# Kernel tuning notes

Hardware: AMD Instinct MI355X
Metric: run time of the kernel (lower is better)

## Reference

```python
import jax, jax.numpy as jnp
import numpy as np

T_STEPS = 30
HIDDEN = 16
INPUT_DIM = 32
OUTPUT_DIM = 1
BATCH = 262144


def setup_inputs() -> dict:
    key = jax.random.key(0)
    ks = jax.random.split(key, 8)
    u = lambda k, shape: jax.random.uniform(k, shape, jnp.float32, -0.25, 0.25)
    return {
        "x": jax.random.normal(ks[0], (BATCH, INPUT_DIM), jnp.float32),
        "T": T_STEPS,
        "W_ih": u(ks[1], (HIDDEN, INPUT_DIM)),
        "W_hh": u(ks[2], (HIDDEN, HIDDEN)),
        "b_ih": u(ks[3], (HIDDEN,)),
        "b_hh": u(ks[4], (HIDDEN,)),
        "W_fc": jax.random.normal(ks[5], (OUTPUT_DIM, HIDDEN), jnp.float32) * 0.25,
        "b_fc": jax.random.normal(ks[6], (OUTPUT_DIM,), jnp.float32) * 0.25,
    }


def reference(x, T, W_ih, W_hh, b_ih, b_hh, W_fc, b_fc):
    # Input is the same at every timestep (x repeated T times), so the
    # input projection is computed once and reused across the scan.
    xproj = x @ W_ih.T + b_ih + b_hh  # [B, H]
    h0 = jnp.zeros((x.shape[0], W_hh.shape[0]), dtype=x.dtype)

    def step(h, _):
        h = jnp.tanh(xproj + h @ W_hh.T)  # Elman: tanh(Wx+b_ih + Uh+b_hh)
        return h, h

    _, hs = jax.lax.scan(step, h0, None, length=T)  # [T, B, H]
    hs = jnp.transpose(hs, (1, 0, 2))               # [B, T, H] (batch_first)
    return hs @ W_fc.T + b_fc                       # [B, T, output_dim]
```

## Files before the change

### kernel.cpp

```cpp
#include <hip/hip_runtime.h>


#define T_STEPS 30
#define BLOCK   256

typedef short v4s __attribute__((ext_vector_type(4)));
typedef float v4f __attribute__((ext_vector_type(4)));
typedef int   v2i __attribute__((ext_vector_type(2)));

__device__ __forceinline__ float tanh_fast(float v) {
    float e = __builtin_amdgcn_exp2f(v * 2.8853900817779268f);
    float r = __builtin_amdgcn_rcpf(1.0f + e);
    return fmaf(-2.0f, r, 1.0f);
}

__device__ __forceinline__ int pack_bf16hi(float a, float b) {
    return (int)__builtin_amdgcn_perm(__float_as_uint(b), __float_as_uint(a),
                                      0x07060302u);
}

__device__ __forceinline__ v4s pack4(float a, float b, float c, float d) {
    v2i p;
    p[0] = pack_bf16hi(a, b);
    p[1] = pack_bf16hi(c, d);
    return __builtin_bit_cast(v4s, p);
}

__device__ __forceinline__ float bf16_trunc_f32(float f) {
    return __uint_as_float(__float_as_uint(f) & 0xFFFF0000u);
}

__global__ __launch_bounds__(BLOCK, 8) void rnn_mfma(
    const float* __restrict__ x,
    const float* __restrict__ W_ih,
    const float* __restrict__ W_hh,
    const float* __restrict__ b_ih,
    const float* __restrict__ b_hh,
    const float* __restrict__ W_fc,
    const float* __restrict__ b_fc,
    float* __restrict__ out)
{
    __shared__ float tmp[64 * T_STEPS];

    const int tid  = threadIdx.x;
    const int w    = tid >> 6;
    const int lane = tid & 63;
    const int r    = lane & 15;
    const int q    = lane >> 4;

    const size_t row = (size_t)blockIdx.x * 64 + (size_t)w * 16 + r;

    const int j0 = 4 * q;
    float xp0 = b_ih[j0 + 0] + b_hh[j0 + 0];
    float xp1 = b_ih[j0 + 1] + b_hh[j0 + 1];
    float xp2 = b_ih[j0 + 2] + b_hh[j0 + 2];
    float xp3 = b_ih[j0 + 3] + b_hh[j0 + 3];
    {
        const float4* xrow = (const float4*)(x + row * 32);
#pragma unroll
        for (int c4 = 0; c4 < 8; ++c4) {
            float4 xv = xrow[c4];
            const float4 w0 = *(const float4*)(W_ih + (j0 + 0) * 32 + c4 * 4);
            const float4 w1 = *(const float4*)(W_ih + (j0 + 1) * 32 + c4 * 4);
            const float4 w2 = *(const float4*)(W_ih + (j0 + 2) * 32 + c4 * 4);
            const float4 w3 = *(const float4*)(W_ih + (j0 + 3) * 32 + c4 * 4);
            xp0 = fmaf(w0.x, xv.x, fmaf(w0.y, xv.y, fmaf(w0.z, xv.z, fmaf(w0.w, xv.w, xp0))));
            xp1 = fmaf(w1.x, xv.x, fmaf(w1.y, xv.y, fmaf(w1.z, xv.z, fmaf(w1.w, xv.w, xp1))));
            xp2 = fmaf(w2.x, xv.x, fmaf(w2.y, xv.y, fmaf(w2.z, xv.z, fmaf(w2.w, xv.w, xp2))));
            xp3 = fmaf(w3.x, xv.x, fmaf(w3.y, xv.y, fmaf(w3.z, xv.z, fmaf(w3.w, xv.w, xp3))));
        }
    }
    const v4f xpv = {xp0, xp1, xp2, xp3};

    v4s whi, wlo;
    {
        float4 wr = *(const float4*)(W_hh + r * 16 + 4 * q);
        float wf[4] = {wr.x, wr.y, wr.z, wr.w};
        whi = pack4(wf[0], wf[1], wf[2], wf[3]);
        wlo = pack4(wf[0] - bf16_trunc_f32(wf[0]), wf[1] - bf16_trunc_f32(wf[1]),
                    wf[2] - bf16_trunc_f32(wf[2]), wf[3] - bf16_trunc_f32(wf[3]));
    }

    v4s afc;
    {
        float f[4];
#pragma unroll
        for (int i = 0; i < 4; ++i) {
            float wv = W_fc[4 * q + i];
            float lo = wv - bf16_trunc_f32(wv);
            f[i] = (r == 0) ? wv : ((r == 1) ? lo : 0.0f);
        }
        afc = pack4(f[0], f[1], f[2], f[3]);
    }

    const float bfc = b_fc[0];
    const v4f zfc = {(q == 0) ? bfc : 0.0f, 0.0f, 0.0f, 0.0f};

    v4s s_hi = {0, 0, 0, 0};
    v4s s_lo = {0, 0, 0, 0};

    float* myout = &tmp[(w * 16 + r) * T_STEPS];

#pragma unroll
    for (int t = 0; t < T_STEPS; ++t) {
        v4f acc = __builtin_amdgcn_mfma_f32_16x16x16bf16_1k(whi, s_hi, xpv, 0, 0, 0);
        acc = __builtin_amdgcn_mfma_f32_16x16x16bf16_1k(whi, s_lo, acc, 0, 0, 0);
        acc = __builtin_amdgcn_mfma_f32_16x16x16bf16_1k(wlo, s_hi, acc, 0, 0, 0);

        float h0 = tanh_fast(acc[0]);
        float h1 = tanh_fast(acc[1]);
        float h2 = tanh_fast(acc[2]);
        float h3 = tanh_fast(acc[3]);
        s_hi = pack4(h0, h1, h2, h3);
        s_lo = pack4(h0 - bf16_trunc_f32(h0), h1 - bf16_trunc_f32(h1),
                     h2 - bf16_trunc_f32(h2), h3 - bf16_trunc_f32(h3));

        v4f facc = __builtin_amdgcn_mfma_f32_16x16x16bf16_1k(afc, s_hi, zfc, 0, 0, 0);
        facc = __builtin_amdgcn_mfma_f32_16x16x16bf16_1k(afc, s_lo, facc, 0, 0, 0);

        if (lane < 16)
            myout[t] = facc[0] + facc[1];
    }

    __syncthreads();

    float* oblk = out + (size_t)blockIdx.x * (64 * T_STEPS);
    for (int idx = tid; idx < 64 * T_STEPS; idx += BLOCK)
        oblk[idx] = tmp[idx];
}

extern "C" void kernel_launch(void* const* d_in, const int* in_sizes, int n_in,
                              void* d_out, int out_size, void* d_ws, size_t ws_size,
                              hipStream_t stream) {
    const float* x    = (const float*)d_in[0];
    const float* W_ih = (const float*)d_in[2];
    const float* W_hh = (const float*)d_in[3];
    const float* b_ih = (const float*)d_in[4];
    const float* b_hh = (const float*)d_in[5];
    const float* W_fc = (const float*)d_in[6];
    const float* b_fc = (const float*)d_in[7];
    float* out = (float*)d_out;

    const int B = in_sizes[0] / 32;
    const int grid = B / 64;

    rnn_mfma<<<grid, BLOCK, 0, stream>>>(x, W_ih, W_hh, b_ih, b_hh, W_fc, b_fc, out);
}
```

Measured before the change: 138.6 us.

## Process two independent 16-row tiles per wave and prescale tanh input

Each wave now runs two independent recurrences (rows A and B), interleaving their MFMA chains to hide MFMA and transcendental latency in the serial time loop. The 2*log2(e) tanh scale is folded into W_hh and the input projection, removing a multiply per element per step. Blocks cover 128 rows, so the grid is halved, LDS doubles, and the copy-out loop is fully unrolled. More registers per thread may reduce occupancy, and scaling before the bf16 split slightly changes rounding.

```diff
diff --git a/kernel.cpp b/kernel.cpp
--- a/kernel.cpp
+++ b/kernel.cpp
@@ -3,13 +3,14 @@
 
 #define T_STEPS 30
 #define BLOCK   256
+#define SCALE   2.8853900817779268f
 
 typedef short v4s __attribute__((ext_vector_type(4)));
 typedef float v4f __attribute__((ext_vector_type(4)));
 typedef int   v2i __attribute__((ext_vector_type(2)));
 
-__device__ __forceinline__ float tanh_fast(float v) {
-    float e = __builtin_amdgcn_exp2f(v * 2.8853900817779268f);
+__device__ __forceinline__ float tanh_pre(float a) {
+    float e = __builtin_amdgcn_exp2f(a);
     float r = __builtin_amdgcn_rcpf(1.0f + e);
     return fmaf(-2.0f, r, 1.0f);
 }
@@ -18,14 +19,12 @@
     return (int)__builtin_amdgcn_perm(__float_as_uint(b), __float_as_uint(a),
                                       0x07060302u);
 }
-
 __device__ __forceinline__ v4s pack4(float a, float b, float c, float d) {
     v2i p;
     p[0] = pack_bf16hi(a, b);
     p[1] = pack_bf16hi(c, d);
     return __builtin_bit_cast(v4s, p);
 }
-
 __device__ __forceinline__ float bf16_trunc_f32(float f) {
     return __uint_as_float(__float_as_uint(f) & 0xFFFF0000u);
 }
@@ -40,42 +39,51 @@
     const float* __restrict__ b_fc,
     float* __restrict__ out)
 {
-    __shared__ float tmp[64 * T_STEPS];
+    __shared__ float tmp[128 * T_STEPS];
 
     const int tid  = threadIdx.x;
     const int w    = tid >> 6;
     const int lane = tid & 63;
     const int r    = lane & 15;
     const int q    = lane >> 4;
+    const int j0   = 4 * q;
 
-    const size_t row = (size_t)blockIdx.x * 64 + (size_t)w * 16 + r;
+    const size_t rowA = (size_t)blockIdx.x * 128 + (size_t)w * 32 + r;
+    const size_t rowB = rowA + 16;
 
-    const int j0 = 4 * q;
-    float xp0 = b_ih[j0 + 0] + b_hh[j0 + 0];
-    float xp1 = b_ih[j0 + 1] + b_hh[j0 + 1];
-    float xp2 = b_ih[j0 + 2] + b_hh[j0 + 2];
-    float xp3 = b_ih[j0 + 3] + b_hh[j0 + 3];
+    float a0 = b_ih[j0 + 0] + b_hh[j0 + 0];
+    float a1 = b_ih[j0 + 1] + b_hh[j0 + 1];
+    float a2 = b_ih[j0 + 2] + b_hh[j0 + 2];
+    float a3 = b_ih[j0 + 3] + b_hh[j0 + 3];
+    float c0 = a0, c1 = a1, c2 = a2, c3 = a3;
     {
-        const float4* xrow = (const float4*)(x + row * 32);
+        const float4* xA = (const float4*)(x + rowA * 32);
+        const float4* xB = (const float4*)(x + rowB * 32);
 #pragma unroll
         for (int c4 = 0; c4 < 8; ++c4) {
-            float4 xv = xrow[c4];
+            float4 xa = xA[c4];
+            float4 xb = xB[c4];
             const float4 w0 = *(const float4*)(W_ih + (j0 + 0) * 32 + c4 * 4);
             const float4 w1 = *(const float4*)(W_ih + (j0 + 1) * 32 + c4 * 4);
             const float4 w2 = *(const float4*)(W_ih + (j0 + 2) * 32 + c4 * 4);
             const float4 w3 = *(const float4*)(W_ih + (j0 + 3) * 32 + c4 * 4);
-            xp0 = fmaf(w0.x, xv.x, fmaf(w0.y, xv.y, fmaf(w0.z, xv.z, fmaf(w0.w, xv.w, xp0))));
-            xp1 = fmaf(w1.x, xv.x, fmaf(w1.y, xv.y, fmaf(w1.z, xv.z, fmaf(w1.w, xv.w, xp1))));
-            xp2 = fmaf(w2.x, xv.x, fmaf(w2.y, xv.y, fmaf(w2.z, xv.z, fmaf(w2.w, xv.w, xp2))));
-            xp3 = fmaf(w3.x, xv.x, fmaf(w3.y, xv.y, fmaf(w3.z, xv.z, fmaf(w3.w, xv.w, xp3))));
+            a0 = fmaf(w0.x, xa.x, fmaf(w0.y, xa.y, fmaf(w0.z, xa.z, fmaf(w0.w, xa.w, a0))));
+            a1 = fmaf(w1.x, xa.x, fmaf(w1.y, xa.y, fmaf(w1.z, xa.z, fmaf(w1.w, xa.w, a1))));
+            a2 = fmaf(w2.x, xa.x, fmaf(w2.y, xa.y, fmaf(w2.z, xa.z, fmaf(w2.w, xa.w, a2))));
+            a3 = fmaf(w3.x, xa.x, fmaf(w3.y, xa.y, fmaf(w3.z, xa.z, fmaf(w3.w, xa.w, a3))));
+            c0 = fmaf(w0.x, xb.x, fmaf(w0.y, xb.y, fmaf(w0.z, xb.z, fmaf(w0.w, xb.w, c0))));
+            c1 = fmaf(w1.x, xb.x, fmaf(w1.y, xb.y, fmaf(w1.z, xb.z, fmaf(w1.w, xb.w, c1))));
+            c2 = fmaf(w2.x, xb.x, fmaf(w2.y, xb.y, fmaf(w2.z, xb.z, fmaf(w2.w, xb.w, c2))));
+            c3 = fmaf(w3.x, xb.x, fmaf(w3.y, xb.y, fmaf(w3.z, xb.z, fmaf(w3.w, xb.w, c3))));
         }
     }
-    const v4f xpv = {xp0, xp1, xp2, xp3};
+    const v4f xpA = {a0 * SCALE, a1 * SCALE, a2 * SCALE, a3 * SCALE};
+    const v4f xpB = {c0 * SCALE, c1 * SCALE, c2 * SCALE, c3 * SCALE};
 
     v4s whi, wlo;
     {
         float4 wr = *(const float4*)(W_hh + r * 16 + 4 * q);
-        float wf[4] = {wr.x, wr.y, wr.z, wr.w};
+        float wf[4] = {wr.x * SCALE, wr.y * SCALE, wr.z * SCALE, wr.w * SCALE};
         whi = pack4(wf[0], wf[1], wf[2], wf[3]);
         wlo = pack4(wf[0] - bf16_trunc_f32(wf[0]), wf[1] - bf16_trunc_f32(wf[1]),
                     wf[2] - bf16_trunc_f32(wf[2]), wf[3] - bf16_trunc_f32(wf[3]));
@@ -92,41 +100,55 @@
         }
         afc = pack4(f[0], f[1], f[2], f[3]);
     }
-
     const float bfc = b_fc[0];
     const v4f zfc = {(q == 0) ? bfc : 0.0f, 0.0f, 0.0f, 0.0f};
 
-    v4s s_hi = {0, 0, 0, 0};
-    v4s s_lo = {0, 0, 0, 0};
+    v4s sAhi = {0, 0, 0, 0}, sAlo = {0, 0, 0, 0};
+    v4s sBhi = {0, 0, 0, 0}, sBlo = {0, 0, 0, 0};
 
-    float* myout = &tmp[(w * 16 + r) * T_STEPS];
+    float* outA = &tmp[(w * 32 + r) * T_STEPS];
+    float* outB = outA + 16 * T_STEPS;
 
 #pragma unroll
     for (int t = 0; t < T_STEPS; ++t) {
-        v4f acc = __builtin_amdgcn_mfma_f32_16x16x16bf16_1k(whi, s_hi, xpv, 0, 0, 0);
-        acc = __builtin_amdgcn_mfma_f32_16x16x16bf16_1k(whi, s_lo, acc, 0, 0, 0);
-        acc = __builtin_amdgcn_mfma_f32_16x16x16bf16_1k(wlo, s_hi, acc, 0, 0, 0);
+        v4f accA = __builtin_amdgcn_mfma_f32_16x16x16bf16_1k(whi, sAhi, xpA, 0, 0, 0);
+        accA = __builtin_amdgcn_mfma_f32_16x16x16bf16_1k(whi, sAlo, accA, 0, 0, 0);
+        accA = __builtin_amdgcn_mfma_f32_16x16x16bf16_1k(wlo, sAhi, accA, 0, 0, 0);
+        v4f accB = __builtin_amdgcn_mfma_f32_16x16x16bf16_1k(whi, sBhi, xpB, 0, 0, 0);
+        accB = __builtin_amdgcn_mfma_f32_16x16x16bf16_1k(whi, sBlo, accB, 0, 0, 0);
+        accB = __builtin_amdgcn_mfma_f32_16x16x16bf16_1k(wlo, sBhi, accB, 0, 0, 0);
 
-        float h0 = tanh_fast(acc[0]);
-        float h1 = tanh_fast(acc[1]);
-        float h2 = tanh_fast(acc[2]);
-        float h3 = tanh_fast(acc[3]);
-        s_hi = pack4(h0, h1, h2, h3);
-        s_lo = pack4(h0 - bf16_trunc_f32(h0), h1 - bf16_trunc_f32(h1),
-                     h2 - bf16_trunc_f32(h2), h3 - bf16_trunc_f32(h3));
+        float hA0 = tanh_pre(accA[0]), hA1 = tanh_pre(accA[1]);
+        float hA2 = tanh_pre(accA[2]), hA3 = tanh_pre(accA[3]);
+        float hB0 = tanh_pre(accB[0]), hB1 = tanh_pre(accB[1]);
+        float hB2 = tanh_pre(accB[2]), hB3 = tanh_pre(accB[3]);
 
-        v4f facc = __builtin_amdgcn_mfma_f32_16x16x16bf16_1k(afc, s_hi, zfc, 0, 0, 0);
-        facc = __builtin_amdgcn_mfma_f32_16x16x16bf16_1k(afc, s_lo, facc, 0, 0, 0);
+        sAhi = pack4(hA0, hA1, hA2, hA3);
+        sAlo = pack4(hA0 - bf16_trunc_f32(hA0), hA1 - bf16_trunc_f32(hA1),
+                     hA2 - bf16_trunc_f32(hA2), hA3 - bf16_trunc_f32(hA3));
+        sBhi = pack4(hB0, hB1, hB2, hB3);
+        sBlo = pack4(hB0 - bf16_trunc_f32(hB0), hB1 - bf16_trunc_f32(hB1),
+                     hB2 - bf16_trunc_f32(hB2), hB3 - bf16_trunc_f32(hB3));
 
-        if (lane < 16)
-            myout[t] = facc[0] + facc[1];
+        v4f fA = __builtin_amdgcn_mfma_f32_16x16x16bf16_1k(afc, sAhi, zfc, 0, 0, 0);
+        fA = __builtin_amdgcn_mfma_f32_16x16x16bf16_1k(afc, sAlo, fA, 0, 0, 0);
+        v4f fB = __builtin_amdgcn_mfma_f32_16x16x16bf16_1k(afc, sBhi, zfc, 0, 0, 0);
+        fB = __builtin_amdgcn_mfma_f32_16x16x16bf16_1k(afc, sBlo, fB, 0, 0, 0);
+
+        if (lane < 16) {
+            outA[t] = fA[0] + fA[1];
+            outB[t] = fB[0] + fB[1];
+        }
     }
 
     __syncthreads();
 
-    float* oblk = out + (size_t)blockIdx.x * (64 * T_STEPS);
-    for (int idx = tid; idx < 64 * T_STEPS; idx += BLOCK)
+    float* oblk = out + (size_t)blockIdx.x * (128 * T_STEPS);
+#pragma unroll
+    for (int k = 0; k < (128 * T_STEPS) / BLOCK; ++k) {
+        int idx = tid + k * BLOCK;
         oblk[idx] = tmp[idx];
+    }
 }
 
 extern "C" void kernel_launch(void* const* d_in, const int* in_sizes, int n_in,
@@ -142,7 +164,7 @@
     float* out = (float*)d_out;
 
     const int B = in_sizes[0] / 32;
-    const int grid = B / 64;
+    const int grid = B / 128;
 
     rnn_mfma<<<grid, BLOCK, 0, stream>>>(x, W_ih, W_hh, b_ih, b_hh, W_fc, b_fc, out);
 }
```

After: 144.3 us. 1.04x slower.
